# Kernel optimization log

Measured on AMD Instinct MI355X. Metric: run time of the kernel, lower is better.

## Reference

```python
import jax, jax.numpy as jnp
import numpy as np

D_STATE = 16; D_MODEL = 256; N_HEADS = 8; N_LAYERS = 4; D_REL = 64
HEALTH = 0
WORLD = (1024.0, 1024.0)
B, T, N = 32, 512, 8
ACTION_DIM = 12


def setup_inputs() -> dict:
    key = jax.random.key(0)
    ks = iter(jax.random.split(key, 48))
    s = 0.02
    def w(shape):
        return jax.random.normal(next(ks), shape, jnp.float32) * s
    inp = dict(
        state=jax.random.normal(next(ks), (B, T, N, D_STATE), jnp.float32),
        pos=jax.random.uniform(next(ks), (B, T, N, 2), jnp.float32),
        vel=jax.random.normal(next(ks), (B, T, N, 2), jnp.float32),
        team_ids=jax.random.randint(next(ks), (B, T, N), 0, 2, jnp.int32),
        alive=jax.random.randint(next(ks), (B, T, N), 0, 2, jnp.int32).astype(bool),
        dead=jnp.zeros((D_STATE,), jnp.float32),
        enc_W1=w((D_STATE, D_MODEL)), enc_b1=jnp.zeros((D_MODEL,), jnp.float32),
        enc_W2=w((D_MODEL, D_MODEL)), enc_b2=jnp.zeros((D_MODEL,), jnp.float32),
        team_emb=w((2, D_MODEL)), ship_emb=w((8, D_MODEL)),
        trunk_W1=w((6, D_REL)), trunk_b1=jnp.zeros((D_REL,), jnp.float32),
        trunk_W2=w((D_REL, D_REL)), trunk_b2=jnp.zeros((D_REL,), jnp.float32),
        adapt_W=w((N_LAYERS, D_REL, N_HEADS)), adapt_b=jnp.zeros((N_LAYERS, N_HEADS), jnp.float32),
        norm_w=jnp.ones((N_LAYERS, D_MODEL), jnp.float32),
        Wq=w((N_LAYERS, D_MODEL, D_MODEL)), bq=jnp.zeros((N_LAYERS, D_MODEL), jnp.float32),
        Wk=w((N_LAYERS, D_MODEL, D_MODEL)), bk=jnp.zeros((N_LAYERS, D_MODEL), jnp.float32),
        Wv=w((N_LAYERS, D_MODEL, D_MODEL)), bv=jnp.zeros((N_LAYERS, D_MODEL), jnp.float32),
        Wo=w((N_LAYERS, D_MODEL, D_MODEL)), bo=jnp.zeros((N_LAYERS, D_MODEL), jnp.float32),
        head_W=w((D_MODEL, ACTION_DIM)), head_b=jnp.zeros((ACTION_DIM,), jnp.float32),
    )
    return inp


def _rms(x, g, eps=1e-6):
    return x * jax.lax.rsqrt(jnp.mean(x * x, axis=-1, keepdims=True) + eps) * g


def reference(state, pos, vel, team_ids, alive, dead,
              enc_W1, enc_b1, enc_W2, enc_b2, team_emb, ship_emb,
              trunk_W1, trunk_b1, trunk_W2, trunk_b2, adapt_W, adapt_b,
              norm_w, Wq, bq, Wk, bk, Wv, bv, Wo, bo, head_W, head_b):
    ws = jnp.asarray(WORLD, state.dtype)
    # replace dead entities' state with learned 'dead' vector
    state = jnp.where(alive[..., None], state, dead)
    # state encoder (MLP)
    h = jax.nn.silu(state @ enc_W1 + enc_b1) @ enc_W2 + enc_b2
    # special embeddings
    h = h + team_emb[team_ids] + ship_emb[jnp.arange(N)]  # ship_emb broadcasts over B,T
    # relational trunk: pairwise toroidal geometry features [B,T,N,N,6]
    p = pos * ws
    rel = p[:, :, :, None, :] - p[:, :, None, :, :]
    rel = rel - jnp.round(rel / ws) * ws  # toroidal wrap
    relv = vel[:, :, :, None, :] - vel[:, :, None, :, :]
    dn = jnp.sqrt(jnp.sum(rel * rel, axis=-1) + 1e-8) / ws[0]
    feats = jnp.concatenate([rel / ws, relv, dn[..., None], 1.0 / (1.0 + dn[..., None])], axis=-1)
    trunk = jax.nn.silu(feats @ trunk_W1 + trunk_b1) @ trunk_W2 + trunk_b2  # [B,T,N,N,D_REL]
    dh = D_MODEL // N_HEADS
    scale = dh ** -0.5
    kmask = alive[:, :, None, None, :]  # mask keys
    x = h
    for i in range(N_LAYERS):
        nx = _rms(x, norm_w[i])
        # adapter: per-layer relational bias [B,T,H,N,N]
        bias = jnp.transpose(trunk @ adapt_W[i] + adapt_b[i], (0, 1, 4, 2, 3))
        q = (nx @ Wq[i] + bq[i]).reshape(B, T, N, N_HEADS, dh)
        k = (nx @ Wk[i] + bk[i]).reshape(B, T, N, N_HEADS, dh)
        v = (nx @ Wv[i] + bv[i]).reshape(B, T, N, N_HEADS, dh)
        sc = jnp.einsum('btihd,btjhd->bthij', q, k) * scale + bias
        sc = jnp.where(kmask, sc, -1e9)
        a = jax.nn.softmax(sc, axis=-1)
        o = jnp.einsum('bthij,btjhd->btihd', a, v).reshape(B, T, N, D_MODEL)
        x = x + o @ Wo[i] + bo[i]
    action_logits = x @ head_W + head_b  # [B,T,N,12]
    return action_logits
```

## Files before the change

### kernel.cpp

```cpp
#include <hip/hip_runtime.h>
#include <cstdint>

#define DEV __device__ __forceinline__

typedef __attribute__((ext_vector_type(8))) short short8;
typedef __attribute__((ext_vector_type(4))) float floatx4;
typedef unsigned short u16;
typedef unsigned int u32;

DEV u16 f2bf(float f) {
    unsigned u = __float_as_uint(f);
    return (u16)((u + 0x7fffu + ((u >> 16) & 1u)) >> 16);
}
DEV void unpack2(u32 u, float& a, float& b) {
    a = __uint_as_float(u << 16);
    b = __uint_as_float(u & 0xffff0000u);
}
DEV u32 pack2f(float a, float b) { return (u32)f2bf(a) | ((u32)f2bf(b) << 16); }
DEV float sigm(float x) { return 1.0f / (1.0f + __expf(-x)); }

#define NAG 8
#define DM 256
#define NL 4
#define AD 12
#define MROWS 32
#define NBLK 4096

#define OFF_E1   0
#define OFF_E2   8192
#define OFF_QKVO 73728
#define OFF_TW2  1122304
#define OFF_ADW  1126400
#define WS_TOTAL 1128448
#define WS_BYTES (WS_TOTAL * 2)

#define L_R1    0
#define L_R2    33792
#define L_RED   50688
#define L_SPOS  51200
#define L_SVEL  51456
#define SMEM_BYTES 51712

#define TRK(row, col) ((row) * 64 + ((((col) >> 3) ^ ((row) & 7)) << 3) + ((col) & 7))

enum { I_STATE=0, I_POS, I_VEL, I_TEAM, I_ALIVE, I_DEAD, I_EW1, I_EB1, I_EW2, I_EB2,
       I_TEMB, I_SEMB, I_TW1, I_TB1, I_TW2, I_TB2, I_ADW, I_ADB, I_NORMW,
       I_WQ, I_BQ, I_WK, I_BK, I_WV, I_BV, I_WO, I_BO, I_HW, I_HB, N_IN };

struct Args { const void* in[N_IN]; float* out; };

__global__ __launch_bounds__(256) void prep_kernel(Args a, u16* ws)
{
    int e = blockIdx.x * 256 + threadIdx.x;
    int mat = blockIdx.y;
    int size, offs, N, Kreal;
    const float* src;
    if (mat == 0)      { size = 8192;  offs = OFF_E1;  N = 256; Kreal = 16;  src = (const float*)a.in[I_EW1]; }
    else if (mat == 1) { size = 65536; offs = OFF_E2;  N = 256; Kreal = 256; src = (const float*)a.in[I_EW2]; }
    else if (mat < 18) {
        int q = mat - 2, l = q >> 2, m = q & 3;
        int wi = (m == 0) ? I_WQ : (m == 1) ? I_WK : (m == 2) ? I_WV : I_WO;
        size = 65536; offs = OFF_QKVO + q * 65536; N = 256; Kreal = 256;
        src = (const float*)a.in[wi] + l * 65536;
    }
    else if (mat == 18) { size = 4096; offs = OFF_TW2; N = 64; Kreal = 64; src = (const float*)a.in[I_TW2]; }
    else                { size = 2048; offs = OFF_ADW; N = 32; Kreal = 64; src = (const float*)a.in[I_ADW]; }
    if (e >= size) return;
    int ksblk = N * 32;
    int ks = e / ksblk, rem = e % ksblk;
    int n = rem >> 5, quad = (rem >> 3) & 3, j = rem & 7;
    int k = ks * 32 + quad * 8 + j;
    float v = 0.0f;
    if (k < Kreal) {
        if (mat == 19) v = src[((n >> 3) * 64 + k) * 8 + (n & 7)];
        else           v = src[k * N + n];
    }
    ws[offs + e] = f2bf(v);
}

DEV short8 ld_u4(const u16* p) {
    union { uint4 u; short8 s; } c;
    c.u = *(const uint4*)p;
    return c.s;
}
DEV short8 ld_afrag(const u16* A, int stride, int row0, int kofs, int l15, int quad) {
    return ld_u4(A + (row0 + l15) * stride + kofs + quad * 8);
}
DEV short8 ld_bws(const u16* w, int ksblk, int ks, int col, int l15, int quad) {
    return ld_u4(w + ks * ksblk + (col + l15) * 32 + quad * 8);
}
DEV short8 ld_bf32(const float* W, int N, int Kreal, int ks, int col, int l15, int quad) {
    short8 r;
    #pragma unroll
    for (int j = 0; j < 8; j++) {
        int k = ks * 32 + quad * 8 + j;
        float v = (k < Kreal) ? W[k * N + col + l15] : 0.0f;
        r[j] = (short)f2bf(v);
    }
    return r;
}

template<bool UW>
DEV void gemm32(const u16* A, const u16* wsW, const float* Wf,
                int Kb, int Kreal, int colw, int l15, int quad, floatx4 acc[2][4]) {
    for (int ks = 0; ks < Kb; ks++) {
        short8 af0 = ld_afrag(A, 264, 0,  ks * 32, l15, quad);
        short8 af1 = ld_afrag(A, 264, 16, ks * 32, l15, quad);
        short8 bf[4];
        #pragma unroll
        for (int nj = 0; nj < 4; nj++)
            bf[nj] = UW ? ld_bws(wsW, 8192, ks, colw + nj * 16, l15, quad)
                        : ld_bf32(Wf, 256, Kreal, ks, colw + nj * 16, l15, quad);
        #pragma unroll
        for (int nj = 0; nj < 4; nj++) {
            acc[0][nj] = __builtin_amdgcn_mfma_f32_16x16x32_bf16(af0, bf[nj], acc[0][nj], 0, 0, 0);
            acc[1][nj] = __builtin_amdgcn_mfma_f32_16x16x32_bf16(af1, bf[nj], acc[1][nj], 0, 0, 0);
        }
    }
}

template<bool UW>
__global__ __launch_bounds__(256, 2) void yemong_mfma(Args a, const u16* ws)
{
    extern __shared__ char smem[];
    u16* sR1   = (u16*)(smem + L_R1);
    u16* skb   = (u16*)(smem + L_R1 + 16896);
    u16* sR2   = (u16*)(smem + L_R2);
    float* sred = (float*)(smem + L_RED);
    float* spos = (float*)(smem + L_SPOS);
    float* svel = (float*)(smem + L_SVEL);

    const int t = threadIdx.x, bid = blockIdx.x;
    const int lane = t & 63, w = t >> 6;
    const int l15 = lane & 15, quad = lane >> 4;
    const int colw = w * 64;
    const int p = w >> 1, h0 = (w & 1) * 4;

    float xr[2][4][4];
    u32 br[NL][4][2];
    u32 amask;

    unsigned mp = 0;
    const unsigned* au = (const unsigned*)a.in[I_ALIVE];
    #pragma unroll
    for (int i = 0; i < 16; i++) mp |= au[i];
    const bool abyte = (mp > 1u);
    auto aliveAt = [&](int r) -> int {
        int gi = bid * MROWS + r;
        return abyte ? (int)((const unsigned char*)a.in[I_ALIVE])[gi]
                     : ((const int*)a.in[I_ALIVE])[gi];
    };

    if (t < 64) {
        int n = t >> 1, d = t & 1;
        spos[n * 2 + d] = ((const float*)a.in[I_POS])[(bid * MROWS + n) * 2 + d] * 1024.0f;
        svel[n * 2 + d] = ((const float*)a.in[I_VEL])[(bid * MROWS + n) * 2 + d];
    }
    {
        int tk = 2 * p + (quad >> 1);
        amask = 0;
        #pragma unroll
        for (int j = 0; j < 8; j++) amask |= (aliveAt(tk * 8 + j) ? 1u : 0u) << j;
    }
    {
        const float* gs = (const float*)a.in[I_STATE];
        const float* gd = (const float*)a.in[I_DEAD];
        #pragma unroll
        for (int it = 0; it < 4; it++) {
            int idx = t + 256 * it;
            int r = idx >> 5, kk = idx & 31;
            float v = 0.0f;
            if (kk < 16) v = aliveAt(r) ? gs[(bid * MROWS + r) * 16 + kk] : gd[kk];
            sR2[r * 264 + kk] = f2bf(v);
        }
    }
    __syncthreads();

    {
        floatx4 acc[2][4] = {};
        gemm32<UW>(sR2, ws + OFF_E1, (const float*)a.in[I_EW1], 1, 16, colw, l15, quad, acc);
        __syncthreads();
        const float* b1 = (const float*)a.in[I_EB1];
        #pragma unroll
        for (int nj = 0; nj < 4; nj++) {
            int c = colw + nj * 16 + l15;
            float bb = b1[c];
            #pragma unroll
            for (int mi = 0; mi < 2; mi++)
                #pragma unroll
                for (int r = 0; r < 4; r++) {
                    float v = acc[mi][nj][r] + bb;
                    sR2[(mi * 16 + quad * 4 + r) * 264 + c] = f2bf(v * sigm(v));
                }
        }
    }
    __syncthreads();

    {
        floatx4 acc[2][4] = {};
        gemm32<UW>(sR2, ws + OFF_E2, (const float*)a.in[I_EW2], 8, 256, colw, l15, quad, acc);
        const float* b2 = (const float*)a.in[I_EB2];
        const float* te = (const float*)a.in[I_TEMB];
        const float* se = (const float*)a.in[I_SEMB];
        const int* gteam = (const int*)a.in[I_TEAM];
        int team8[8];
        #pragma unroll
        for (int mi = 0; mi < 2; mi++)
            #pragma unroll
            for (int r = 0; r < 4; r++)
                team8[mi * 4 + r] = gteam[bid * MROWS + mi * 16 + quad * 4 + r];
        #pragma unroll
        for (int nj = 0; nj < 4; nj++) {
            int c = colw + nj * 16 + l15;
            float bb = b2[c];
            #pragma unroll
            for (int mi = 0; mi < 2; mi++)
                #pragma unroll
                for (int r = 0; r < 4; r++) {
                    int row = mi * 16 + quad * 4 + r;
                    xr[mi][nj][r] = acc[mi][nj][r] + bb + te[team8[mi * 4 + r] * 256 + c] + se[(row & 7) * 256 + c];
                }
        }
    }

    {
        int tokp = t >> 6;
        int pi = tokp * 8 + ((t >> 3) & 7), pj = tokp * 8 + (t & 7);
        float rx = spos[pi * 2 + 0] - spos[pj * 2 + 0];
        float ry = spos[pi * 2 + 1] - spos[pj * 2 + 1];
        rx -= rintf(rx * (1.0f / 1024.0f)) * 1024.0f;
        ry -= rintf(ry * (1.0f / 1024.0f)) * 1024.0f;
        float vx = svel[pi * 2 + 0] - svel[pj * 2 + 0];
        float vy = svel[pi * 2 + 1] - svel[pj * 2 + 1];
        float dn = sqrtf(rx * rx + ry * ry + 1e-8f) * (1.0f / 1024.0f);
        float f[6] = {rx * (1.0f / 1024.0f), ry * (1.0f / 1024.0f), vx, vy, dn, 1.0f / (1.0f + dn)};
        const float* W1 = (const float*)a.in[I_TW1];
        const float* B1 = (const float*)a.in[I_TB1];
        #pragma unroll
        for (int g = 0; g < 8; g++) {
            float v[8];
            #pragma unroll
            for (int e = 0; e < 8; e++) v[e] = B1[g * 8 + e];
            #pragma unroll
            for (int kk = 0; kk < 6; kk++)
                #pragma unroll
                for (int e = 0; e < 8; e++) v[e] = fmaf(f[kk], W1[kk * 64 + g * 8 + e], v[e]);
            #pragma unroll
            for (int e = 0; e < 8; e++) v[e] = v[e] * sigm(v[e]);
            uint4 pk;
            pk.x = pack2f(v[0], v[1]); pk.y = pack2f(v[2], v[3]);
            pk.z = pack2f(v[4], v[5]); pk.w = pack2f(v[6], v[7]);
            *(uint4*)&sR1[t * 64 + ((g ^ (t & 7)) << 3)] = pk;
        }
    }
    __syncthreads();

    {
        short8 taf[4][2];
        #pragma unroll
        for (int mi = 0; mi < 4; mi++)
            #pragma unroll
            for (int ks = 0; ks < 2; ks++) {
                int R = colw + mi * 16 + l15;
                taf[mi][ks] = ld_u4(&sR1[R * 64 + (((ks * 4 + quad) ^ (R & 7)) << 3)]);
            }
        floatx4 tacc[4][4] = {};
        #pragma unroll
        for (int ks = 0; ks < 2; ks++) {
            short8 bf[4];
            #pragma unroll
            for (int nj = 0; nj < 4; nj++)
                bf[nj] = UW ? ld_bws(ws + OFF_TW2, 2048, ks, nj * 16, l15, quad)
                            : ld_bf32((const float*)a.in[I_TW2], 64, 64, ks, nj * 16, l15, quad);
            #pragma unroll
            for (int mi = 0; mi < 4; mi++)
                #pragma unroll
                for (int nj = 0; nj < 4; nj++)
                    tacc[mi][nj] = __builtin_amdgcn_mfma_f32_16x16x32_bf16(taf[mi][ks], bf[nj], tacc[mi][nj], 0, 0, 0);
        }
        const float* B2 = (const float*)a.in[I_TB2];
        #pragma unroll
        for (int nj = 0; nj < 4; nj++) {
            int c = nj * 16 + l15;
            float bb = B2[c];
            #pragma unroll
            for (int mi = 0; mi < 4; mi++)
                #pragma unroll
                for (int r = 0; r < 4; r++) {
                    int row = colw + mi * 16 + quad * 4 + r;
                    sR1[TRK(row, c)] = f2bf(tacc[mi][nj][r] + bb);
                }
        }
    }
    __syncthreads();

    {
        floatx4 tacc[4][2] = {};
        #pragma unroll
        for (int ks = 0; ks < 2; ks++) {
            short8 bf[2];
            #pragma unroll
            for (int nj = 0; nj < 2; nj++) {
                if (UW) bf[nj] = ld_bws(ws + OFF_ADW, 1024, ks, nj * 16, l15, quad);
                else {
                    const float* adw = (const float*)a.in[I_ADW];
                    int n = nj * 16 + l15;
                    #pragma unroll
                    for (int j = 0; j < 8; j++) {
                        int k = ks * 32 + quad * 8 + j;
                        bf[nj][j] = (short)f2bf(k < 64 ? adw[((n >> 3) * 64 + k) * 8 + (n & 7)] : 0.0f);
                    }
                }
            }
            #pragma unroll
            for (int mi = 0; mi < 4; mi++) {
                int R = colw + mi * 16 + l15;
                short8 af = ld_u4(&sR1[R * 64 + (((ks * 4 + quad) ^ (R & 7)) << 3)]);
                #pragma unroll
                for (int nj = 0; nj < 2; nj++)
                    tacc[mi][nj] = __builtin_amdgcn_mfma_f32_16x16x32_bf16(af, bf[nj], tacc[mi][nj], 0, 0, 0);
            }
        }
        const float* adb = (const float*)a.in[I_ADB];
        #pragma unroll
        for (int nj = 0; nj < 2; nj++) {
            int n = nj * 16 + l15;
            float bb = adb[n];
            #pragma unroll
            for (int mi = 0; mi < 4; mi++)
                #pragma unroll
                for (int r = 0; r < 4; r++) {
                    int pl = mi * 16 + quad * 4 + r;
                    sR2[((w * 4 + (n >> 3)) * 8 + (n & 7)) * 64 + pl] = f2bf(tacc[mi][nj][r] + bb);
                }
        }
        __syncthreads();
        int tk = 2 * p + (quad >> 1);
        #pragma unroll
        for (int l = 0; l < NL; l++)
            #pragma unroll
            for (int u = 0; u < 4; u++) {
                int base = ((tk * 4 + l) * 8 + (h0 + u)) * 64 + (l15 & 7) * 8 + (quad & 1) * 4;
                const u32* bp = (const u32*)&sR2[base];
                br[l][u][0] = bp[0];
                br[l][u][1] = bp[1];
            }
    }
    __syncthreads();

    const float* normw = (const float*)a.in[I_NORMW];
    const bool qvalid = ((quad >> 1) == (l15 >> 3));
    #pragma unroll
    for (int l = 0; l < NL; l++) {
        float invr[8];
        {
            float ssv[8];
            #pragma unroll
            for (int mi = 0; mi < 2; mi++)
                #pragma unroll
                for (int r = 0; r < 4; r++) {
                    float s = 0.0f;
                    #pragma unroll
                    for (int nj = 0; nj < 4; nj++) { float v = xr[mi][nj][r]; s = fmaf(v, v, s); }
                    ssv[mi * 4 + r] = s;
                }
            #pragma unroll
            for (int m = 1; m < 16; m <<= 1)
                #pragma unroll
                for (int k2 = 0; k2 < 8; k2++) ssv[k2] += __shfl_xor(ssv[k2], m);
            if (l15 == 0) {
                #pragma unroll
                for (int mi = 0; mi < 2; mi++)
                    #pragma unroll
                    for (int r = 0; r < 4; r++)
                        sred[(mi * 16 + quad * 4 + r) * 4 + w] = ssv[mi * 4 + r];
            }
            __syncthreads();
            #pragma unroll
            for (int mi = 0; mi < 2; mi++)
                #pragma unroll
                for (int r = 0; r < 4; r++) {
                    int row = mi * 16 + quad * 4 + r;
                    float s = sred[row * 4 + 0] + sred[row * 4 + 1] + sred[row * 4 + 2] + sred[row * 4 + 3];
                    invr[mi * 4 + r] = rsqrtf(s * (1.0f / 256.0f) + 1e-6f);
                }
        }
        {
            #pragma unroll
            for (int nj = 0; nj < 4; nj++) {
                int c = colw + nj * 16 + l15;
                float nwv = normw[l * 256 + c];
                #pragma unroll
                for (int mi = 0; mi < 2; mi++)
                    #pragma unroll
                    for (int r = 0; r < 4; r++)
                        sR2[(mi * 16 + quad * 4 + r) * 264 + c] = f2bf(xr[mi][nj][r] * invr[mi * 4 + r] * nwv);
            }
        }
        __syncthreads();

        {
            floatx4 acc[3][2][4] = {};
            const u16* wq  = ws + OFF_QKVO + (l * 4 + 0) * 65536;
            const u16* wk  = ws + OFF_QKVO + (l * 4 + 1) * 65536;
            const u16* wvv = ws + OFF_QKVO + (l * 4 + 2) * 65536;
            const float* fq = (const float*)a.in[I_WQ] + l * 65536;
            const float* fk = (const float*)a.in[I_WK] + l * 65536;
            const float* fv = (const float*)a.in[I_WV] + l * 65536;
            #pragma unroll 2
            for (int ks = 0; ks < 8; ks++) {
                short8 af0 = ld_afrag(sR2, 264, 0,  ks * 32, l15, quad);
                short8 af1 = ld_afrag(sR2, 264, 16, ks * 32, l15, quad);
                short8 bq[4], bk[4], bv[4];
                #pragma unroll
                for (int nj = 0; nj < 4; nj++) {
                    int c = colw + nj * 16;
                    bq[nj] = UW ? ld_bws(wq,  8192, ks, c, l15, quad) : ld_bf32(fq, 256, 256, ks, c, l15, quad);
                    bk[nj] = UW ? ld_bws(wk,  8192, ks, c, l15, quad) : ld_bf32(fk, 256, 256, ks, c, l15, quad);
                    bv[nj] = UW ? ld_bws(wvv, 8192, ks, c, l15, quad) : ld_bf32(fv, 256, 256, ks, c, l15, quad);
                }
                #pragma unroll
                for (int nj = 0; nj < 4; nj++) {
                    acc[0][0][nj] = __builtin_amdgcn_mfma_f32_16x16x32_bf16(af0, bq[nj], acc[0][0][nj], 0, 0, 0);
                    acc[0][1][nj] = __builtin_amdgcn_mfma_f32_16x16x32_bf16(af1, bq[nj], acc[0][1][nj], 0, 0, 0);
                    acc[1][0][nj] = __builtin_amdgcn_mfma_f32_16x16x32_bf16(af0, bk[nj], acc[1][0][nj], 0, 0, 0);
                    acc[1][1][nj] = __builtin_amdgcn_mfma_f32_16x16x32_bf16(af1, bk[nj], acc[1][1][nj], 0, 0, 0);
                    acc[2][0][nj] = __builtin_amdgcn_mfma_f32_16x16x32_bf16(af0, bv[nj], acc[2][0][nj], 0, 0, 0);
                    acc[2][1][nj] = __builtin_amdgcn_mfma_f32_16x16x32_bf16(af1, bv[nj], acc[2][1][nj], 0, 0, 0);
                }
            }
            const float* bqf = (const float*)a.in[I_BQ] + l * 256;
            const float* bkf = (const float*)a.in[I_BK] + l * 256;
            #pragma unroll
            for (int nj = 0; nj < 4; nj++) {
                int c = colw + nj * 16 + l15;
                float b0 = bqf[c], b1 = bkf[c];
                #pragma unroll
                for (int mi = 0; mi < 2; mi++)
                    #pragma unroll
                    for (int r = 0; r < 4; r++) {
                        int row = mi * 16 + quad * 4 + r;
                        sR1[row * 264 + c] = f2bf((acc[0][mi][nj][r] + b0) * 0.17677669529663689f);
                        skb[row * 264 + c] = f2bf(acc[1][mi][nj][r] + b1);
                    }
            }
            __syncthreads();
            const float* bvf = (const float*)a.in[I_BV] + l * 256;
            #pragma unroll
            for (int nj = 0; nj < 4; nj++) {
                int c = colw + nj * 16 + l15;
                float b2v = bvf[c];
                #pragma unroll
                for (int mi = 0; mi < 2; mi++)
                    #pragma unroll
                    for (int r = 0; r < 4; r++)
                        sR2[(mi * 16 + quad * 4 + r) * 264 + c] = f2bf(acc[2][mi][nj][r] + b2v);
            }
        }
        __syncthreads();

        #pragma unroll
        for (int u = 0; u < 4; u++) {
            int h = h0 + u;
            short8 kf = ld_u4(&skb[(p * 16 + l15) * 264 + h * 32 + quad * 8]);
            short8 qf = ld_u4(&sR1[(p * 16 + l15) * 264 + h * 32 + quad * 8]);
            floatx4 zero = {};
            floatx4 st = __builtin_amdgcn_mfma_f32_16x16x32_bf16(kf, qf, zero, 0, 0, 0);
            float bb[4];
            unpack2(br[l][u][0], bb[0], bb[1]);
            unpack2(br[l][u][1], bb[2], bb[3]);
            float s[4];
            #pragma unroll
            for (int r = 0; r < 4; r++) {
                int jl = (quad & 1) * 4 + r;
                bool alv = (amask >> jl) & 1;
                s[r] = qvalid ? (alv ? st[r] + bb[r] : -1.0e9f) : -2.0e9f;
            }
            float mx = fmaxf(fmaxf(s[0], s[1]), fmaxf(s[2], s[3]));
            mx = fmaxf(mx, __shfl_xor(mx, 16));
            mx = fmaxf(mx, __shfl_xor(mx, 32));
            float e[4], sm = 0.0f;
            #pragma unroll
            for (int r = 0; r < 4; r++) { e[r] = __expf(s[r] - mx); sm += e[r]; }
            sm += __shfl_xor(sm, 16);
            sm += __shfl_xor(sm, 32);
            float inv = 1.0f / sm;
            u32 u01 = pack2f(e[0] * inv, e[1] * inv);
            u32 u23 = pack2f(e[2] * inv, e[3] * inv);
            int srcA = (quad * 32 + l15) & 63;
            u32 a0 = (u32)__shfl((int)u01, srcA);
            u32 a1 = (u32)__shfl((int)u23, srcA);
            u32 a2 = (u32)__shfl((int)u01, (srcA + 16) & 63);
            u32 a3 = (u32)__shfl((int)u23, (srcA + 16) & 63);
            if (quad >= 2) { a0 = 0; a1 = 0; a2 = 0; a3 = 0; }
            union { u32 uu[4]; short8 ss; } cv;
            cv.uu[0] = a0; cv.uu[1] = a1; cv.uu[2] = a2; cv.uu[3] = a3;
            short8 paf = cv.ss;
            #pragma unroll
            for (int nt = 0; nt < 2; nt++) {
                short8 vf;
                if (quad < 2) {
                    #pragma unroll
                    for (int jj = 0; jj < 8; jj++) {
                        int kr = quad * 8 + jj;
                        vf[jj] = (short)sR2[(p * 16 + kr) * 264 + h * 32 + nt * 16 + l15];
                    }
                } else {
                    #pragma unroll
                    for (int jj = 0; jj < 8; jj++) vf[jj] = 0;
                }
                floatx4 z2 = {};
                floatx4 o = __builtin_amdgcn_mfma_f32_16x16x32_bf16(paf, vf, z2, 0, 0, 0);
                #pragma unroll
                for (int r = 0; r < 4; r++)
                    sR1[(p * 16 + quad * 4 + r) * 264 + h * 32 + nt * 16 + l15] = f2bf(o[r]);
            }
        }
        __syncthreads();

        {
            floatx4 acc[2][4] = {};
            gemm32<UW>(sR1, ws + OFF_QKVO + (l * 4 + 3) * 65536, (const float*)a.in[I_WO] + l * 65536,
                       8, 256, colw, l15, quad, acc);
            const float* bo = (const float*)a.in[I_BO] + l * 256;
            #pragma unroll
            for (int nj = 0; nj < 4; nj++) {
                float bb = bo[colw + nj * 16 + l15];
                #pragma unroll
                for (int mi = 0; mi < 2; mi++)
                    #pragma unroll
                    for (int r = 0; r < 4; r++)
                        xr[mi][nj][r] += acc[mi][nj][r] + bb;
            }
        }
        __syncthreads();
    }

    {
        float* xf = (float*)sR1;
        #pragma unroll
        for (int nj = 0; nj < 4; nj++) {
            int c = colw + nj * 16 + l15;
            #pragma unroll
            for (int mi = 0; mi < 2; mi++)
                #pragma unroll
                for (int r = 0; r < 4; r++)
                    xf[(mi * 16 + quad * 4 + r) * 264 + c] = xr[mi][nj][r];
        }
        __syncthreads();
        int row = t >> 3, pp = t & 7;
        const float* HW = (const float*)a.in[I_HW];
        float ah[12];
        #pragma unroll
        for (int c = 0; c < 12; c++) ah[c] = 0.0f;
        for (int kk = pp * 32; kk < pp * 32 + 32; kk++) {
            float xv = xf[row * 264 + kk];
            #pragma unroll
            for (int c = 0; c < 12; c++) ah[c] = fmaf(xv, HW[kk * 12 + c], ah[c]);
        }
        #pragma unroll
        for (int c = 0; c < 12; c++) {
            ah[c] += __shfl_xor(ah[c], 1);
            ah[c] += __shfl_xor(ah[c], 2);
            ah[c] += __shfl_xor(ah[c], 4);
        }
        if (pp == 0) {
            const float* hb = (const float*)a.in[I_HB];
            #pragma unroll
            for (int c = 0; c < 12; c++)
                a.out[(bid * MROWS + row) * AD + c] = ah[c] + hb[c];
        }
    }
}

extern "C" void kernel_launch(void* const* d_in, const int* in_sizes, int n_in,
                              void* d_out, int out_size, void* d_ws, size_t ws_size,
                              hipStream_t stream) {
    (void)in_sizes; (void)n_in; (void)out_size;
    Args a;
    for (int i = 0; i < N_IN; i++) a.in[i] = d_in[i];
    a.out = (float*)d_out;
    u16* ws16 = (u16*)d_ws;
    const bool use_ws = (ws_size >= (size_t)WS_BYTES) && (d_ws != nullptr);
    if (use_ws) {
        hipLaunchKernelGGL(prep_kernel, dim3(256, 20), dim3(256), 0, stream, a, ws16);
        hipFuncSetAttribute((const void*)yemong_mfma<true>, hipFuncAttributeMaxDynamicSharedMemorySize, SMEM_BYTES);
        hipLaunchKernelGGL((yemong_mfma<true>), dim3(NBLK), dim3(256), SMEM_BYTES, stream, a, ws16);
    } else {
        hipFuncSetAttribute((const void*)yemong_mfma<false>, hipFuncAttributeMaxDynamicSharedMemorySize, SMEM_BYTES);
        hipLaunchKernelGGL((yemong_mfma<false>), dim3(NBLK), dim3(256), SMEM_BYTES, stream, a, ws16);
    }
}
```

Before: 1.134 ms.

## Separate V buffer, batch per-head attention, and hoist RMS partials to cut barriers

Adds a dedicated shared-memory V buffer so Q, K and V can all be written in one pass before a single barrier, instead of writing V after an extra sync. The RMS-norm partial sums are computed right after each residual update and reuse the barrier that already follows it, which removes another barrier per layer. Attention now loads all head fragments and issues the score MFMAs for the four heads together before the softmax, giving more independent work to hide latency. In exchange, shared memory per block grows from about 51 KB to about 68 KB, which could limit how many blocks fit on a CU.

```diff
diff --git a/kernel.cpp b/kernel.cpp
--- a/kernel.cpp
+++ b/kernel.cpp
@@ -35,11 +35,13 @@
 #define WS_BYTES (WS_TOTAL * 2)
 
 #define L_R1    0
-#define L_R2    33792
-#define L_RED   50688
-#define L_SPOS  51200
-#define L_SVEL  51456
-#define SMEM_BYTES 51712
+#define L_KB    16896
+#define L_V     33792
+#define L_R2    50688
+#define L_RED   67584
+#define L_SPOS  68096
+#define L_SVEL  68352
+#define SMEM_BYTES 68608
 
 #define TRK(row, col) ((row) * 64 + ((((col) >> 3) ^ ((row) & 7)) << 3) + ((col) & 7))
 
@@ -79,9 +81,7 @@
 }
 
 DEV short8 ld_u4(const u16* p) {
-    union { uint4 u; short8 s; } c;
-    c.u = *(const uint4*)p;
-    return c.s;
+    return __builtin_bit_cast(short8, *(const uint4*)p);
 }
 DEV short8 ld_afrag(const u16* A, int stride, int row0, int kofs, int l15, int quad) {
     return ld_u4(A + (row0 + l15) * stride + kofs + quad * 8);
@@ -124,7 +124,8 @@
 {
     extern __shared__ char smem[];
     u16* sR1   = (u16*)(smem + L_R1);
-    u16* skb   = (u16*)(smem + L_R1 + 16896);
+    u16* skb   = (u16*)(smem + L_KB);
+    u16* sV    = (u16*)(smem + L_V);
     u16* sR2   = (u16*)(smem + L_R2);
     float* sred = (float*)(smem + L_RED);
     float* spos = (float*)(smem + L_SPOS);
@@ -150,6 +151,29 @@
         return abyte ? (int)((const unsigned char*)a.in[I_ALIVE])[gi]
                      : ((const int*)a.in[I_ALIVE])[gi];
     };
+    auto rms_partials = [&]() {
+        float ssv[8];
+        #pragma unroll
+        for (int mi = 0; mi < 2; mi++)
+            #pragma unroll
+            for (int r = 0; r < 4; r++) {
+                float s = 0.0f;
+                #pragma unroll
+                for (int nj = 0; nj < 4; nj++) { float v = xr[mi][nj][r]; s = fmaf(v, v, s); }
+                ssv[mi * 4 + r] = s;
+            }
+        #pragma unroll
+        for (int m = 1; m < 16; m <<= 1)
+            #pragma unroll
+            for (int k2 = 0; k2 < 8; k2++) ssv[k2] += __shfl_xor(ssv[k2], m);
+        if (l15 == 0) {
+            #pragma unroll
+            for (int mi = 0; mi < 2; mi++)
+                #pragma unroll
+                for (int r = 0; r < 4; r++)
+                    sred[(mi * 16 + quad * 4 + r) * 4 + w] = ssv[mi * 4 + r];
+        }
+    };
 
     if (t < 64) {
         int n = t >> 1, d = t & 1;
@@ -221,6 +245,7 @@
                     xr[mi][nj][r] = acc[mi][nj][r] + bb + te[team8[mi * 4 + r] * 256 + c] + se[(row & 7) * 256 + c];
                 }
         }
+        rms_partials();
     }
 
     {
@@ -352,30 +377,8 @@
     const bool qvalid = ((quad >> 1) == (l15 >> 3));
     #pragma unroll
     for (int l = 0; l < NL; l++) {
-        float invr[8];
         {
-            float ssv[8];
-            #pragma unroll
-            for (int mi = 0; mi < 2; mi++)
-                #pragma unroll
-                for (int r = 0; r < 4; r++) {
-                    float s = 0.0f;
-                    #pragma unroll
-                    for (int nj = 0; nj < 4; nj++) { float v = xr[mi][nj][r]; s = fmaf(v, v, s); }
-                    ssv[mi * 4 + r] = s;
-                }
-            #pragma unroll
-            for (int m = 1; m < 16; m <<= 1)
-                #pragma unroll
-                for (int k2 = 0; k2 < 8; k2++) ssv[k2] += __shfl_xor(ssv[k2], m);
-            if (l15 == 0) {
-                #pragma unroll
-                for (int mi = 0; mi < 2; mi++)
-                    #pragma unroll
-                    for (int r = 0; r < 4; r++)
-                        sred[(mi * 16 + quad * 4 + r) * 4 + w] = ssv[mi * 4 + r];
-            }
-            __syncthreads();
+            float invr[8];
             #pragma unroll
             for (int mi = 0; mi < 2; mi++)
                 #pragma unroll
@@ -384,8 +387,6 @@
                     float s = sred[row * 4 + 0] + sred[row * 4 + 1] + sred[row * 4 + 2] + sred[row * 4 + 3];
                     invr[mi * 4 + r] = rsqrtf(s * (1.0f / 256.0f) + 1e-6f);
                 }
-        }
-        {
             #pragma unroll
             for (int nj = 0; nj < 4; nj++) {
                 int c = colw + nj * 16 + l15;
@@ -431,10 +432,11 @@
             }
             const float* bqf = (const float*)a.in[I_BQ] + l * 256;
             const float* bkf = (const float*)a.in[I_BK] + l * 256;
+            const float* bvf = (const float*)a.in[I_BV] + l * 256;
             #pragma unroll
             for (int nj = 0; nj < 4; nj++) {
                 int c = colw + nj * 16 + l15;
-                float b0 = bqf[c], b1 = bkf[c];
+                float b0 = bqf[c], b1 = bkf[c], b2v = bvf[c];
                 #pragma unroll
                 for (int mi = 0; mi < 2; mi++)
                     #pragma unroll
@@ -442,78 +444,81 @@
                         int row = mi * 16 + quad * 4 + r;
                         sR1[row * 264 + c] = f2bf((acc[0][mi][nj][r] + b0) * 0.17677669529663689f);
                         skb[row * 264 + c] = f2bf(acc[1][mi][nj][r] + b1);
+                        sV [row * 264 + c] = f2bf(acc[2][mi][nj][r] + b2v);
                     }
             }
-            __syncthreads();
-            const float* bvf = (const float*)a.in[I_BV] + l * 256;
-            #pragma unroll
-            for (int nj = 0; nj < 4; nj++) {
-                int c = colw + nj * 16 + l15;
-                float b2v = bvf[c];
-                #pragma unroll
-                for (int mi = 0; mi < 2; mi++)
+        }
+        __syncthreads();
+
+        {
+            short8 kf[4], qf[4];
+            #pragma unroll
+            for (int u = 0; u < 4; u++) {
+                int h = h0 + u;
+                kf[u] = ld_u4(&skb[(p * 16 + l15) * 264 + h * 32 + quad * 8]);
+                qf[u] = ld_u4(&sR1[(p * 16 + l15) * 264 + h * 32 + quad * 8]);
+            }
+            floatx4 st[4];
+            #pragma unroll
+            for (int u = 0; u < 4; u++) {
+                floatx4 zero = {};
+                st[u] = __builtin_amdgcn_mfma_f32_16x16x32_bf16(kf[u], qf[u], zero, 0, 0, 0);
+            }
+            short8 paf[4];
+            #pragma unroll
+            for (int u = 0; u < 4; u++) {
+                float bb[4];
+                unpack2(br[l][u][0], bb[0], bb[1]);
+                unpack2(br[l][u][1], bb[2], bb[3]);
+                float s[4];
+                #pragma unroll
+                for (int r = 0; r < 4; r++) {
+                    int jl = (quad & 1) * 4 + r;
+                    bool alv = (amask >> jl) & 1;
+                    s[r] = qvalid ? (alv ? st[u][r] + bb[r] : -1.0e9f) : -2.0e9f;
+                }
+                float mx = fmaxf(fmaxf(s[0], s[1]), fmaxf(s[2], s[3]));
+                mx = fmaxf(mx, __shfl_xor(mx, 16));
+                mx = fmaxf(mx, __shfl_xor(mx, 32));
+                float e[4], sm = 0.0f;
+                #pragma unroll
+                for (int r = 0; r < 4; r++) { e[r] = __expf(s[r] - mx); sm += e[r]; }
+                sm += __shfl_xor(sm, 16);
+                sm += __shfl_xor(sm, 32);
+                float inv = 1.0f / sm;
+                u32 u01 = pack2f(e[0] * inv, e[1] * inv);
+                u32 u23 = pack2f(e[2] * inv, e[3] * inv);
+                int srcA = (quad * 32 + l15) & 63;
+                u32 a0 = (u32)__shfl((int)u01, srcA);
+                u32 a1 = (u32)__shfl((int)u23, srcA);
+                u32 a2 = (u32)__shfl((int)u01, (srcA + 16) & 63);
+                u32 a3 = (u32)__shfl((int)u23, (srcA + 16) & 63);
+                if (quad >= 2) { a0 = 0; a1 = 0; a2 = 0; a3 = 0; }
+                uint4 tmp; tmp.x = a0; tmp.y = a1; tmp.z = a2; tmp.w = a3;
+                paf[u] = __builtin_bit_cast(short8, tmp);
+            }
+            #pragma unroll
+            for (int u = 0; u < 4; u++) {
+                int h = h0 + u;
+                #pragma unroll
+                for (int nt = 0; nt < 2; nt++) {
+                    short8 vf;
+                    if (quad < 2) {
+                        #pragma unroll
+                        for (int jj = 0; jj < 8; jj++) {
+                            int kr = quad * 8 + jj;
+                            vf[jj] = (short)sV[(p * 16 + kr) * 264 + h * 32 + nt * 16 + l15];
+                        }
+                    } else {
+                        #pragma unroll
+                        for (int jj = 0; jj < 8; jj++) vf[jj] = 0;
+                    }
+                    floatx4 z2 = {};
+                    floatx4 o = __builtin_amdgcn_mfma_f32_16x16x32_bf16(paf[u], vf, z2, 0, 0, 0);
                     #pragma unroll
                     for (int r = 0; r < 4; r++)
-                        sR2[(mi * 16 + quad * 4 + r) * 264 + c] = f2bf(acc[2][mi][nj][r] + b2v);
-            }
-        }
-        __syncthreads();
-
-        #pragma unroll
-        for (int u = 0; u < 4; u++) {
-            int h = h0 + u;
-            short8 kf = ld_u4(&skb[(p * 16 + l15) * 264 + h * 32 + quad * 8]);
-            short8 qf = ld_u4(&sR1[(p * 16 + l15) * 264 + h * 32 + quad * 8]);
-            floatx4 zero = {};
-            floatx4 st = __builtin_amdgcn_mfma_f32_16x16x32_bf16(kf, qf, zero, 0, 0, 0);
-            float bb[4];
-            unpack2(br[l][u][0], bb[0], bb[1]);
-            unpack2(br[l][u][1], bb[2], bb[3]);
-            float s[4];
-            #pragma unroll
-            for (int r = 0; r < 4; r++) {
-                int jl = (quad & 1) * 4 + r;
-                bool alv = (amask >> jl) & 1;
-                s[r] = qvalid ? (alv ? st[r] + bb[r] : -1.0e9f) : -2.0e9f;
-            }
-            float mx = fmaxf(fmaxf(s[0], s[1]), fmaxf(s[2], s[3]));
-            mx = fmaxf(mx, __shfl_xor(mx, 16));
-            mx = fmaxf(mx, __shfl_xor(mx, 32));
-            float e[4], sm = 0.0f;
-            #pragma unroll
-            for (int r = 0; r < 4; r++) { e[r] = __expf(s[r] - mx); sm += e[r]; }
-            sm += __shfl_xor(sm, 16);
-            sm += __shfl_xor(sm, 32);
-            float inv = 1.0f / sm;
-            u32 u01 = pack2f(e[0] * inv, e[1] * inv);
-            u32 u23 = pack2f(e[2] * inv, e[3] * inv);
-            int srcA = (quad * 32 + l15) & 63;
-            u32 a0 = (u32)__shfl((int)u01, srcA);
-            u32 a1 = (u32)__shfl((int)u23, srcA);
-            u32 a2 = (u32)__shfl((int)u01, (srcA + 16) & 63);
-            u32 a3 = (u32)__shfl((int)u23, (srcA + 16) & 63);
-            if (quad >= 2) { a0 = 0; a1 = 0; a2 = 0; a3 = 0; }
-            union { u32 uu[4]; short8 ss; } cv;
-            cv.uu[0] = a0; cv.uu[1] = a1; cv.uu[2] = a2; cv.uu[3] = a3;
-            short8 paf = cv.ss;
-            #pragma unroll
-            for (int nt = 0; nt < 2; nt++) {
-                short8 vf;
-                if (quad < 2) {
-                    #pragma unroll
-                    for (int jj = 0; jj < 8; jj++) {
-                        int kr = quad * 8 + jj;
-                        vf[jj] = (short)sR2[(p * 16 + kr) * 264 + h * 32 + nt * 16 + l15];
-                    }
-                } else {
-                    #pragma unroll
-                    for (int jj = 0; jj < 8; jj++) vf[jj] = 0;
-                }
-                floatx4 z2 = {};
-                floatx4 o = __builtin_amdgcn_mfma_f32_16x16x32_bf16(paf, vf, z2, 0, 0, 0);
-                #pragma unroll
-                for (int r = 0; r < 4; r++)
-                    sR1[(p * 16 + quad * 4 + r) * 264 + h * 32 + nt * 16 + l15] = f2bf(o[r]);
+                        sR1[(p * 16 + quad * 4 + r) * 264 + h * 32 + nt * 16 + l15] = f2bf(o[r]);
+                }
             }
         }
         __syncthreads();
@@ -532,6 +537,7 @@
                     for (int r = 0; r < 4; r++)
                         xr[mi][nj][r] += acc[mi][nj][r] + bb;
             }
+            rms_partials();
         }
         __syncthreads();
     }
```

Measured after the change: 1.124 ms. No clear change (-0.9%).
